# Kernel tuning notes

Hardware: AMD Instinct MI355X
Metric: run time of the kernel (lower is better)

Reference implementation:

```python
import jax, jax.numpy as jnp
import numpy as np

S, M, E = 8192, 4096, 64          # tokens, model_dim, num_experts
CAPACITY_FACTOR = 1.0
MIN_CAPACITY = 8
CAPACITY = max(int(np.ceil(S / E * CAPACITY_FACTOR)), MIN_CAPACITY)  # 128


def setup_inputs() -> dict:
    key = jax.random.key(0)
    k1, k2 = jax.random.split(key)
    x = jax.random.normal(k1, (S, M), dtype=jnp.float32)
    wg = jax.random.normal(k2, (E, M), dtype=jnp.float32) * (1.0 / np.sqrt(M))
    return {"x": x, "wg": wg}


def reference(x, wg):
    # gate projection (Linear, no bias): logits [s, e]
    logits = jnp.einsum('sm,em->se', x, wg)
    gates = jax.nn.softmax(logits, axis=1)                      # [s, e]

    # top-1 expert per token
    indices1_s = jnp.argmax(gates, axis=1)                      # [s]
    mask1 = jax.nn.one_hot(indices1_s, E, dtype=jnp.int32)      # [s, e]
    exp_counts = jnp.sum(mask1, axis=0)                         # [e]

    # load-balancing aux loss
    me = jnp.mean(gates, axis=0)
    ce = jnp.mean(mask1.astype(jnp.float32), axis=0)
    l_aux = jnp.sum(me * ce) * E

    # capacity drop (use_rts=False): keep first CAPACITY tokens per expert.
    # torch: top_idx = topk(mask1, capacity, dim=0)[1]; scatter ones at those rows.
    top_idx = jax.lax.top_k(mask1.T, CAPACITY)[1]               # [e, c] token ids
    keep = jnp.zeros((S, E), dtype=jnp.int32).at[top_idx.T, jnp.arange(E)[None, :]].set(1)
    mask1 = mask1 * keep                                        # [s, e]

    # position of each token inside its expert's buffer
    locations1 = jnp.cumsum(mask1, axis=0) - 1                  # [s, e]
    locations1_s = jnp.sum(locations1 * mask1, axis=1)          # [s]

    mask1_f = mask1.astype(gates.dtype)
    gates_masked = gates * mask1_f                              # [s, e]
    locations1_sc = jax.nn.one_hot(locations1_s, CAPACITY, dtype=jnp.float32)  # [s, c]

    combine_weights = jnp.einsum('se,sc->sec', gates_masked, locations1_sc)    # [s, e, c]
    dispatch_mask = combine_weights.astype(bool)
    return l_aux, combine_weights, dispatch_mask, exp_counts
```

## Files before the change

kernel.cpp:

```cpp
#include <hip/hip_runtime.h>
#include <hip/hip_bf16.h>

#define TS 8192
#define TM 4096
#define TE 64
#define TCAP 128
static const size_t CW = (size_t)TS * TE * TCAP;

#define BM 256
#define BK 16
#define SA 260
#define SW 68

__global__ __launch_bounds__(256) void gemm_partial(
    const float* __restrict__ x, const float* __restrict__ wg,
    float* __restrict__ part, int kchunk) {
  __shared__ float As[BK][SA];
  __shared__ float Ws[BK][SW];
  const int tid = threadIdx.x;
  const int t0 = blockIdx.x * BM;
  const int k0 = blockIdx.y * kchunk;
  const int ntile = kchunk / BK;
  const int tg = tid >> 3;
  const int eg = tid & 7;

  float acc[8][8] = {};
  float4 ra[4]; float4 rw;

  auto load_tile = [&](int kt) {
    const int kb = k0 + kt * BK;
#pragma unroll
    for (int i = 0; i < 4; i++) {
      int idx = tid + 256 * i;
      int tok = idx >> 2, c4 = idx & 3;
      ra[i] = *(const float4*)&x[(size_t)(t0 + tok) * TM + kb + 4 * c4];
    }
    int e = tid >> 2, c4 = tid & 3;
    rw = *(const float4*)&wg[(size_t)e * TM + kb + 4 * c4];
  };

  load_tile(0);
  for (int kt = 0; kt < ntile; kt++) {
#pragma unroll
    for (int i = 0; i < 4; i++) {
      int idx = tid + 256 * i;
      int tok = idx >> 2, c4 = idx & 3;
      As[4 * c4 + 0][tok] = ra[i].x; As[4 * c4 + 1][tok] = ra[i].y;
      As[4 * c4 + 2][tok] = ra[i].z; As[4 * c4 + 3][tok] = ra[i].w;
    }
    { int e = tid >> 2, c4 = tid & 3;
      Ws[4 * c4 + 0][e] = rw.x; Ws[4 * c4 + 1][e] = rw.y;
      Ws[4 * c4 + 2][e] = rw.z; Ws[4 * c4 + 3][e] = rw.w; }
    __syncthreads();
    if (kt + 1 < ntile) load_tile(kt + 1);
#pragma unroll
    for (int k = 0; k < BK; k++) {
      float4 a0 = *(const float4*)&As[k][tg * 8];
      float4 a1 = *(const float4*)&As[k][tg * 8 + 4];
      float4 b0 = *(const float4*)&Ws[k][eg * 8];
      float4 b1 = *(const float4*)&Ws[k][eg * 8 + 4];
      float av[8] = {a0.x, a0.y, a0.z, a0.w, a1.x, a1.y, a1.z, a1.w};
      float bv[8] = {b0.x, b0.y, b0.z, b0.w, b1.x, b1.y, b1.z, b1.w};
#pragma unroll
      for (int i = 0; i < 8; i++)
#pragma unroll
        for (int j = 0; j < 8; j++) acc[i][j] += av[i] * bv[j];
    }
    __syncthreads();
  }
  float* dst = part + (size_t)blockIdx.y * TS * TE;
#pragma unroll
  for (int i = 0; i < 8; i++) {
    int tok = t0 + tg * 8 + i;
#pragma unroll
    for (int j = 0; j < 8; j += 4) {
      float4 v = make_float4(acc[i][j], acc[i][j + 1], acc[i][j + 2], acc[i][j + 3]);
      *(float4*)&dst[(size_t)tok * TE + eg * 8 + j] = v;
    }
  }
}

__global__ __launch_bounds__(256) void softmax_top1(
    const float* __restrict__ part, int KS,
    float* __restrict__ gates, float* __restrict__ gate1, int* __restrict__ idx1) {
  const int s = blockIdx.x * 4 + (threadIdx.x >> 6);
  const int lane = threadIdx.x & 63;
  float logit = 0.0f;
  for (int p = 0; p < KS; p++)
    logit += part[((size_t)p * TS + s) * TE + lane];

  float mv = logit; int mi = lane;
#pragma unroll
  for (int off = 32; off; off >>= 1) {
    float ov = __shfl_xor(mv, off);
    int oi = __shfl_xor(mi, off);
    if (ov > mv || (ov == mv && oi < mi)) { mv = ov; mi = oi; }
  }
  float ex = expf(logit - mv);
  float sum = ex;
#pragma unroll
  for (int off = 32; off; off >>= 1) sum += __shfl_xor(sum, off);
  float g = ex / sum;
  gates[(size_t)s * TE + lane] = g;
  if (lane == mi) { gate1[s] = g; idx1[s] = mi; }
}

__global__ __launch_bounds__(256) void me_reduce(const float* __restrict__ gates,
                                                 float* __restrict__ me) {
  const int e = blockIdx.x, tid = threadIdx.x;
  float s = 0.0f;
  for (int t = tid; t < TS; t += 256) s += gates[(size_t)t * TE + e];
  __shared__ float red[256];
  red[tid] = s; __syncthreads();
  for (int o = 128; o; o >>= 1) { if (tid < o) red[tid] += red[tid + o]; __syncthreads(); }
  if (tid == 0) me[e] = red[0];
}

__global__ void capacity_rank(const int* __restrict__ idx1,
                              int* __restrict__ pos, int* __restrict__ counts) {
  const int e = blockIdx.x, lane = threadIdx.x;
  int base = 0;
  for (int c = 0; c < TS / 64; c++) {
    int s = c * 64 + lane;
    bool m = (idx1[s] == e);
    unsigned long long mask = __ballot(m);
    if (m) {
      int p = base + __popcll(mask & ((1ull << lane) - 1ull));
      pos[s] = (p < TCAP) ? p : -1;
    }
    base += __popcll(mask);
  }
  if (lane == 0) counts[e] = base;
}

__global__ void finalize_laux(const float* __restrict__ me, const int* __restrict__ counts,
                              float* __restrict__ out, size_t cw) {
  const int lane = threadIdx.x;
  float v = (me[lane] / (float)TS) * ((float)counts[lane] / (float)TS);
  float sum = v;
#pragma unroll
  for (int off = 32; off; off >>= 1) sum += __shfl_xor(sum, off);
  if (lane == 0) out[0] = sum * (float)TE;
  out[1 + 2 * cw + lane] = (float)counts[lane];
}

__global__ __launch_bounds__(256) void scatter_out(
    const float* __restrict__ gate1, const int* __restrict__ idx1,
    const int* __restrict__ pos, float* __restrict__ out, size_t cw) {
  const int s = blockIdx.x * 256 + threadIdx.x;
  int p = pos[s];
  if (p >= 0) {
    size_t off = 1 + ((size_t)s * TE + idx1[s]) * (size_t)TCAP + (size_t)p;
    out[off] = gate1[s];
    out[off + cw] = 1.0f;
  }
}

extern "C" void kernel_launch(void* const* d_in, const int* in_sizes, int n_in,
                              void* d_out, int out_size, void* d_ws, size_t ws_size,
                              hipStream_t stream) {
  const float* x = (const float*)d_in[0];
  const float* wg = (const float*)d_in[1];
  float* out = (float*)d_out;

  const size_t SE = (size_t)TS * TE;
  int KS = 8;
  auto need = [&](int ks) {
    return (size_t)ks * SE * 4 + SE * 4 + (size_t)TS * 12 + 1024;
  };
  while (KS > 1 && need(KS) > ws_size) KS >>= 1;

  float* part  = (float*)d_ws;
  float* gates = part + (size_t)KS * SE;
  float* gate1 = gates + SE;
  int*   idx1  = (int*)(gate1 + TS);
  int*   pos   = idx1 + TS;
  float* me    = (float*)(pos + TS);
  int*   cnts  = (int*)(me + TE);

  hipMemsetAsync(d_out, 0, (size_t)out_size * sizeof(float), stream);

  dim3 ggrid(TS / BM, KS);
  gemm_partial<<<ggrid, 256, 0, stream>>>(x, wg, part, TM / KS);
  softmax_top1<<<TS / 4, 256, 0, stream>>>(part, KS, gates, gate1, idx1);
  me_reduce<<<TE, 256, 0, stream>>>(gates, me);
  capacity_rank<<<TE, 64, 0, stream>>>(idx1, pos, cnts);
  finalize_laux<<<1, 64, 0, stream>>>(me, cnts, out, CW);
  scatter_out<<<TS / 256, 256, 0, stream>>>(gate1, idx1, pos, out, CW);
}
```

Before: 697.9 us.

## Fuse output zero-fill into GEMM launch and fold gate mean into softmax

Replaces the separate memset of the large output buffer with fill blocks that run in the same grid as the gate GEMM, interleaved by a block-index permutation so zeroing overlaps with the compute blocks. The GEMM tile shrinks to 128 tokens to give more blocks. The softmax kernel now accumulates the per-expert gate means with atomics, which drops the full gates buffer and the me_reduce kernel. The finalize and scatter kernels are merged into one launch. The split-K factor is now fixed at 8, so the old workspace-size fallback is gone.

Measured after the change: 717.5 us. 2.8% more time.

```diff
diff --git a/kernel.cpp b/kernel.cpp
--- a/kernel.cpp
+++ b/kernel.cpp
@@ -5,44 +5,66 @@
 #define TM 4096
 #define TE 64
 #define TCAP 128
-static const size_t CW = (size_t)TS * TE * TCAP;
+#define KS 8
+#define KCHUNK (TM / KS)
+#define BK 16
+#define NTILE (KCHUNK / BK)
+#define BM 128
+#define GEMM_BLOCKS 512
+#define K1_GRID 2048
+#define NFILL (K1_GRID - GEMM_BLOCKS)
 
-#define BM 256
-#define BK 16
-#define SA 260
-#define SW 68
+constexpr size_t CWsz = (size_t)TS * TE * TCAP;
+constexpr size_t NOUT = 1 + 2 * CWsz + TE;
+constexpr size_t NF4  = (NOUT - 1) / 4;
 
-__global__ __launch_bounds__(256) void gemm_partial(
+__global__ __launch_bounds__(256) void k1_fill_gemm(
     const float* __restrict__ x, const float* __restrict__ wg,
-    float* __restrict__ part, int kchunk) {
-  __shared__ float As[BK][SA];
-  __shared__ float Ws[BK][SW];
+    float* __restrict__ part, float* __restrict__ me, float* __restrict__ out) {
   const int tid = threadIdx.x;
-  const int t0 = blockIdx.x * BM;
-  const int k0 = blockIdx.y * kchunk;
-  const int ntile = kchunk / BK;
+  const int v = (blockIdx.x * 5) & (K1_GRID - 1);
+
+  __shared__ float As[BK][132];
+  __shared__ float Ws[BK][68];
+
+  if (v >= GEMM_BLOCKS) {
+    const int fid = v - GEMM_BLOCKS;
+    const float4 z = make_float4(0.f, 0.f, 0.f, 0.f);
+    float4* o4 = (float4*)out;
+    for (size_t i = (size_t)fid * 256 + tid; i < NF4; i += (size_t)NFILL * 256)
+      o4[i] = z;
+    if (fid == 0) {
+      if (tid == 0) out[NOUT - 1] = 0.0f;
+      if (tid < TE) me[tid] = 0.0f;
+    }
+    return;
+  }
+
+  const int gid = v;
+  const int t0 = (gid & 63) * BM;
+  const int k0 = (gid >> 6) * KCHUNK;
   const int tg = tid >> 3;
   const int eg = tid & 7;
 
-  float acc[8][8] = {};
-  float4 ra[4]; float4 rw;
+  float acc[4][8] = {};
+  float4 ra[2], rw;
 
-  auto load_tile = [&](int kt) {
+  auto load = [&](int kt) {
     const int kb = k0 + kt * BK;
 #pragma unroll
-    for (int i = 0; i < 4; i++) {
+    for (int i = 0; i < 2; i++) {
       int idx = tid + 256 * i;
       int tok = idx >> 2, c4 = idx & 3;
       ra[i] = *(const float4*)&x[(size_t)(t0 + tok) * TM + kb + 4 * c4];
     }
-    int e = tid >> 2, c4 = tid & 3;
-    rw = *(const float4*)&wg[(size_t)e * TM + kb + 4 * c4];
+    { int e = tid >> 2, c4 = tid & 3;
+      rw = *(const float4*)&wg[(size_t)e * TM + kb + 4 * c4]; }
   };
 
-  load_tile(0);
-  for (int kt = 0; kt < ntile; kt++) {
+  load(0);
+  for (int kt = 0; kt < NTILE; kt++) {
 #pragma unroll
-    for (int i = 0; i < 4; i++) {
+    for (int i = 0; i < 2; i++) {
       int idx = tid + 256 * i;
       int tok = idx >> 2, c4 = idx & 3;
       As[4 * c4 + 0][tok] = ra[i].x; As[4 * c4 + 1][tok] = ra[i].y;
@@ -52,72 +74,68 @@
       Ws[4 * c4 + 0][e] = rw.x; Ws[4 * c4 + 1][e] = rw.y;
       Ws[4 * c4 + 2][e] = rw.z; Ws[4 * c4 + 3][e] = rw.w; }
     __syncthreads();
-    if (kt + 1 < ntile) load_tile(kt + 1);
+    if (kt + 1 < NTILE) load(kt + 1);
 #pragma unroll
     for (int k = 0; k < BK; k++) {
-      float4 a0 = *(const float4*)&As[k][tg * 8];
-      float4 a1 = *(const float4*)&As[k][tg * 8 + 4];
+      float4 a  = *(const float4*)&As[k][tg * 4];
       float4 b0 = *(const float4*)&Ws[k][eg * 8];
       float4 b1 = *(const float4*)&Ws[k][eg * 8 + 4];
-      float av[8] = {a0.x, a0.y, a0.z, a0.w, a1.x, a1.y, a1.z, a1.w};
+      float av[4] = {a.x, a.y, a.z, a.w};
       float bv[8] = {b0.x, b0.y, b0.z, b0.w, b1.x, b1.y, b1.z, b1.w};
 #pragma unroll
-      for (int i = 0; i < 8; i++)
+      for (int i = 0; i < 4; i++)
 #pragma unroll
         for (int j = 0; j < 8; j++) acc[i][j] += av[i] * bv[j];
     }
     __syncthreads();
   }
-  float* dst = part + (size_t)blockIdx.y * TS * TE;
+  float* dst = part + (size_t)(gid >> 6) * TS * TE;
 #pragma unroll
-  for (int i = 0; i < 8; i++) {
-    int tok = t0 + tg * 8 + i;
-#pragma unroll
-    for (int j = 0; j < 8; j += 4) {
-      float4 v = make_float4(acc[i][j], acc[i][j + 1], acc[i][j + 2], acc[i][j + 3]);
-      *(float4*)&dst[(size_t)tok * TE + eg * 8 + j] = v;
-    }
+  for (int i = 0; i < 4; i++) {
+    int tok = t0 + tg * 4 + i;
+    *(float4*)&dst[(size_t)tok * TE + eg * 8] =
+        make_float4(acc[i][0], acc[i][1], acc[i][2], acc[i][3]);
+    *(float4*)&dst[(size_t)tok * TE + eg * 8 + 4] =
+        make_float4(acc[i][4], acc[i][5], acc[i][6], acc[i][7]);
   }
 }
 
-__global__ __launch_bounds__(256) void softmax_top1(
-    const float* __restrict__ part, int KS,
-    float* __restrict__ gates, float* __restrict__ gate1, int* __restrict__ idx1) {
-  const int s = blockIdx.x * 4 + (threadIdx.x >> 6);
-  const int lane = threadIdx.x & 63;
-  float logit = 0.0f;
-  for (int p = 0; p < KS; p++)
-    logit += part[((size_t)p * TS + s) * TE + lane];
-
-  float mv = logit; int mi = lane;
+__global__ __launch_bounds__(256) void k2_softmax(
+    const float* __restrict__ part, float* __restrict__ gate1,
+    int* __restrict__ idx1, float* __restrict__ me) {
+  const int tid = threadIdx.x, w = tid >> 6, lane = tid & 63;
+  const int s0 = blockIdx.x * 32;
+  float mesum = 0.0f;
+  for (int it = 0; it < 8; it++) {
+    const int s = s0 + it * 4 + w;
+    float logit = 0.0f;
 #pragma unroll
-  for (int off = 32; off; off >>= 1) {
-    float ov = __shfl_xor(mv, off);
-    int oi = __shfl_xor(mi, off);
-    if (ov > mv || (ov == mv && oi < mi)) { mv = ov; mi = oi; }
+    for (int p = 0; p < KS; p++)
+      logit += part[((size_t)p * TS + s) * TE + lane];
+    float mv = logit; int mi = lane;
+#pragma unroll
+    for (int off = 32; off; off >>= 1) {
+      float ov = __shfl_xor(mv, off);
+      int oi = __shfl_xor(mi, off);
+      if (ov > mv || (ov == mv && oi < mi)) { mv = ov; mi = oi; }
+    }
+    float ex = expf(logit - mv);
+    float sum = ex;
+#pragma unroll
+    for (int off = 32; off; off >>= 1) sum += __shfl_xor(sum, off);
+    float g = ex / sum;
+    mesum += g;
+    if (lane == mi) { gate1[s] = g; idx1[s] = mi; }
   }
-  float ex = expf(logit - mv);
-  float sum = ex;
-#pragma unroll
-  for (int off = 32; off; off >>= 1) sum += __shfl_xor(sum, off);
-  float g = ex / sum;
-  gates[(size_t)s * TE + lane] = g;
-  if (lane == mi) { gate1[s] = g; idx1[s] = mi; }
+  __shared__ float red[4][64];
+  red[w][lane] = mesum;
+  __syncthreads();
+  if (w == 0)
+    atomicAdd(&me[lane], red[0][lane] + red[1][lane] + red[2][lane] + red[3][lane]);
 }
 
-__global__ __launch_bounds__(256) void me_reduce(const float* __restrict__ gates,
-                                                 float* __restrict__ me) {
-  const int e = blockIdx.x, tid = threadIdx.x;
-  float s = 0.0f;
-  for (int t = tid; t < TS; t += 256) s += gates[(size_t)t * TE + e];
-  __shared__ float red[256];
-  red[tid] = s; __syncthreads();
-  for (int o = 128; o; o >>= 1) { if (tid < o) red[tid] += red[tid + o]; __syncthreads(); }
-  if (tid == 0) me[e] = red[0];
-}
-
-__global__ void capacity_rank(const int* __restrict__ idx1,
-                              int* __restrict__ pos, int* __restrict__ counts) {
+__global__ void k3_rank(const int* __restrict__ idx1,
+                        int* __restrict__ pos, int* __restrict__ counts) {
   const int e = blockIdx.x, lane = threadIdx.x;
   int base = 0;
   for (int c = 0; c < TS / 64; c++) {
@@ -133,58 +151,47 @@
   if (lane == 0) counts[e] = base;
 }
 
-__global__ void finalize_laux(const float* __restrict__ me, const int* __restrict__ counts,
-                              float* __restrict__ out, size_t cw) {
-  const int lane = threadIdx.x;
-  float v = (me[lane] / (float)TS) * ((float)counts[lane] / (float)TS);
-  float sum = v;
+__global__ __launch_bounds__(256) void k4_final(
+    const float* __restrict__ gate1, const int* __restrict__ idx1,
+    const int* __restrict__ pos, const float* __restrict__ me,
+    const int* __restrict__ cnts, float* __restrict__ out) {
+  if (blockIdx.x == 32) {
+    if (threadIdx.x < 64) {
+      const int lane = threadIdx.x;
+      float vv = (me[lane] / (float)TS) * ((float)cnts[lane] / (float)TS);
+      float sum = vv;
 #pragma unroll
-  for (int off = 32; off; off >>= 1) sum += __shfl_xor(sum, off);
-  if (lane == 0) out[0] = sum * (float)TE;
-  out[1 + 2 * cw + lane] = (float)counts[lane];
-}
-
-__global__ __launch_bounds__(256) void scatter_out(
-    const float* __restrict__ gate1, const int* __restrict__ idx1,
-    const int* __restrict__ pos, float* __restrict__ out, size_t cw) {
+      for (int off = 32; off; off >>= 1) sum += __shfl_xor(sum, off);
+      if (lane == 0) out[0] = sum * (float)TE;
+      out[1 + 2 * CWsz + lane] = (float)cnts[lane];
+    }
+    return;
+  }
   const int s = blockIdx.x * 256 + threadIdx.x;
-  int p = pos[s];
+  const int p = pos[s];
   if (p >= 0) {
     size_t off = 1 + ((size_t)s * TE + idx1[s]) * (size_t)TCAP + (size_t)p;
     out[off] = gate1[s];
-    out[off + cw] = 1.0f;
+    out[off + CWsz] = 1.0f;
   }
 }
 
 extern "C" void kernel_launch(void* const* d_in, const int* in_sizes, int n_in,
                               void* d_out, int out_size, void* d_ws, size_t ws_size,
                               hipStream_t stream) {
-  const float* x = (const float*)d_in[0];
+  const float* x  = (const float*)d_in[0];
   const float* wg = (const float*)d_in[1];
   float* out = (float*)d_out;
 
-  const size_t SE = (size_t)TS * TE;
-  int KS = 8;
-  auto need = [&](int ks) {
-    return (size_t)ks * SE * 4 + SE * 4 + (size_t)TS * 12 + 1024;
-  };
-  while (KS > 1 && need(KS) > ws_size) KS >>= 1;
-
   float* part  = (float*)d_ws;
-  float* gates = part + (size_t)KS * SE;
-  float* gate1 = gates + SE;
+  float* gate1 = part + (size_t)KS * TS * TE;
   int*   idx1  = (int*)(gate1 + TS);
   int*   pos   = idx1 + TS;
   float* me    = (float*)(pos + TS);
   int*   cnts  = (int*)(me + TE);
 
-  hipMemsetAsync(d_out, 0, (size_t)out_size * sizeof(float), stream);
-
-  dim3 ggrid(TS / BM, KS);
-  gemm_partial<<<ggrid, 256, 0, stream>>>(x, wg, part, TM / KS);
-  softmax_top1<<<TS / 4, 256, 0, stream>>>(part, KS, gates, gate1, idx1);
-  me_reduce<<<TE, 256, 0, stream>>>(gates, me);
-  capacity_rank<<<TE, 64, 0, stream>>>(idx1, pos, cnts);
-  finalize_laux<<<1, 64, 0, stream>>>(me, cnts, out, CW);
-  scatter_out<<<TS / 256, 256, 0, stream>>>(gate1, idx1, pos, out, CW);
+  k1_fill_gemm<<<K1_GRID, 256, 0, stream>>>(x, wg, part, me, out);
+  k2_softmax<<<TS / 32, 256, 0, stream>>>(part, gate1, idx1, me);
+  k3_rank<<<TE, 64, 0, stream>>>(idx1, pos, cnts);
+  k4_final<<<33, 256, 0, stream>>>(gate1, idx1, pos, me, cnts, out);
 }
```
